# Optimization experiments

Measured on AMD Instinct MI355X. Metric: run time of the kernel, lower is better.

## Reference

```python
import jax, jax.numpy as jnp
import numpy as np

N = 16384
D = 512
NNZ = 163840
NUM_ITERS = 10


def setup_inputs() -> dict:
    key = jax.random.key(0)
    k1, k2, k3, k4 = jax.random.split(key, 4)
    x = jax.random.normal(k1, (N, D), dtype=jnp.float32)
    edge_val = jax.random.uniform(k2, (NNZ,), dtype=jnp.float32)
    edge_row = jnp.sort(jax.random.randint(k3, (NNZ,), 0, N, dtype=jnp.int32))
    edge_col = jax.random.randint(k4, (NNZ,), 0, N, dtype=jnp.int32)
    alpha = jnp.zeros((1,), dtype=jnp.float32)
    beta = jnp.zeros((1,), dtype=jnp.float32)
    sigma = jnp.ones((1,), dtype=jnp.float32)
    return {"x": x, "alpha": alpha, "beta": beta, "sigma": sigma,
            "edge_val": edge_val, "edge_row": edge_row, "edge_col": edge_col,
            "num_iters": NUM_ITERS}


def reference(x, alpha, beta, sigma, edge_val, edge_row, edge_col, num_iters):
    n = x.shape[0]
    # tf.nn.l2_normalize(x, axis=1)
    xn = x * jax.lax.rsqrt(jnp.maximum(jnp.sum(x * x, axis=1, keepdims=True), 1e-12))
    # cosine similarity only at sparse support positions; diagonal zeroed
    sim_e = jnp.sum(xn[edge_row] * xn[edge_col], axis=-1)          # [nnz]
    sim_e = jnp.where(edge_row == edge_col, 0.0, sim_e)
    s = jnp.exp(sigma[0])
    sigma_sq = 2.0 * s * s
    sim_e = jnp.exp(sim_e / (2.0 * sigma_sq))
    # support = sparse support elementwise * similarity
    sup = edge_val * sim_e                                          # [nnz]
    # row-sum of sparse support
    normalize = jax.ops.segment_sum(sup, edge_row, num_segments=n)  # [N]
    a = jnp.exp(alpha[0])
    b = jnp.exp(beta[0])
    denom = b + normalize[:, None] * a + a                          # [N,1] -> broadcast over D

    def step(out, _):
        # sparse matmul: (support @ out)
        Ax = jax.ops.segment_sum(sup[:, None] * out[edge_col], edge_row, num_segments=n)
        out = (x * b + (Ax + out) * a) / denom
        return out, None

    out, _ = jax.lax.scan(step, x, None, length=num_iters)
    return out
```

## Files before the change

kernel.cpp:

```cpp
#include <hip/hip_runtime.h>
#include <hip/hip_fp16.h>

#define DIM 512
#define N_ITERS 10

typedef float floatx2 __attribute__((ext_vector_type(2)));
typedef float fx4 __attribute__((ext_vector_type(4)));
typedef unsigned int ux2 __attribute__((ext_vector_type(2)));
typedef unsigned int ux4 __attribute__((ext_vector_type(4)));

__device__ __forceinline__ unsigned int pack2h(float lo, float hi) {
    __half2 h = __float22half2_rn(make_float2(lo, hi));
    return *reinterpret_cast<unsigned int*>(&h);
}
__device__ __forceinline__ float2 unpack2h(unsigned int u) {
    return __half22float2(*reinterpret_cast<__half2*>(&u));
}
__device__ __forceinline__ unsigned int pack4f8(float f0, float f1, float f2, float f3) {
    int v = 0;
    v = __builtin_amdgcn_cvt_pk_fp8_f32(f0, f1, v, false);
    v = __builtin_amdgcn_cvt_pk_fp8_f32(f2, f3, v, true);
    return (unsigned int)v;
}

__global__ void __launch_bounds__(256)
prep_kernel(const float* __restrict__ x,
            const float* __restrict__ alpha,
            const float* __restrict__ beta,
            const float* __restrict__ sigma,
            const int* __restrict__ erow, int nnz,
            float* __restrict__ consts,
            int* __restrict__ rstart,
            unsigned int* __restrict__ xn8,
            float* __restrict__ norms,
            unsigned short* __restrict__ xbh, int n) {
    int tid = blockIdx.x * blockDim.x + threadIdx.x;
    float b = expf(beta[0]);
    if (tid == 0) {
        float a = expf(alpha[0]);
        float s = expf(sigma[0]);
        consts[0] = a;
        consts[1] = b;
        consts[2] = 1.0f / (4.0f * s * s);
    }
    if (tid <= n) {
        int lo = 0, hi = nnz;
        while (lo < hi) {
            int mid = (lo + hi) >> 1;
            if (erow[mid] < tid) lo = mid + 1; else hi = mid;
        }
        rstart[tid] = lo;
    }
    int wid = tid >> 6;
    int lane = tid & 63;
    if (wid >= n) return;
    const size_t base = (size_t)wid * DIM + lane * 8;
    const fx4* p = (const fx4*)(x + base);
    fx4 u = p[0];
    fx4 v = p[1];
    float s = u.x*u.x + u.y*u.y + u.z*u.z + u.w*u.w
            + v.x*v.x + v.y*v.y + v.z*v.z + v.w*v.w;
    ux4 hb;
    hb.x = pack2h(u.x * b, u.y * b); hb.y = pack2h(u.z * b, u.w * b);
    hb.z = pack2h(v.x * b, v.y * b); hb.w = pack2h(v.z * b, v.w * b);
    *(ux4*)(xbh + base) = hb;
    #pragma unroll
    for (int m = 32; m >= 1; m >>= 1) s += __shfl_xor(s, m, 64);
    float inr = rsqrtf(fmaxf(s, 1e-12f));
    if (lane == 0) norms[wid] = s * inr;
    ux2 qn;
    qn.x = pack4f8(u.x * inr, u.y * inr, u.z * inr, u.w * inr);
    qn.y = pack4f8(v.x * inr, v.y * inr, v.z * inr, v.w * inr);
    *(ux2*)(xn8 + ((size_t)wid * (DIM / 4) + lane * 2)) = qn;
}

__device__ __forceinline__ float dot8f8(const float* A, unsigned int lo, unsigned int hi) {
    floatx2 p0 = __builtin_amdgcn_cvt_pk_f32_fp8((int)lo, false);
    floatx2 p1 = __builtin_amdgcn_cvt_pk_f32_fp8((int)lo, true);
    floatx2 p2 = __builtin_amdgcn_cvt_pk_f32_fp8((int)hi, false);
    floatx2 p3 = __builtin_amdgcn_cvt_pk_f32_fp8((int)hi, true);
    return A[0]*p0.x + A[1]*p0.y + A[2]*p1.x + A[3]*p1.y
         + A[4]*p2.x + A[5]*p2.y + A[6]*p3.x + A[7]*p3.y;
}

#define ACCP(lo, hi, w2)                                                          \
    do {                                                                          \
        acc0 += (w2) * __builtin_amdgcn_cvt_pk_f32_fp8((int)(lo), false);         \
        acc1 += (w2) * __builtin_amdgcn_cvt_pk_f32_fp8((int)(lo), true);          \
        acc2 += (w2) * __builtin_amdgcn_cvt_pk_f32_fp8((int)(hi), false);         \
        acc3 += (w2) * __builtin_amdgcn_cvt_pk_f32_fp8((int)(hi), true);          \
    } while (0)

__global__ void __launch_bounds__(256)
fused1_kernel(const unsigned int* __restrict__ xn8,
              const float* __restrict__ norms,
              const float* __restrict__ eval_,
              const int* __restrict__ ecol,
              const int* __restrict__ rstart,
              const float* __restrict__ consts,
              float* __restrict__ sup, float* __restrict__ inv_denom,
              const unsigned short* __restrict__ xbh,
              unsigned short* __restrict__ next16,
              unsigned int* __restrict__ next8, int n) {
    int row = (blockIdx.x * blockDim.x + threadIdx.x) >> 6;
    int lane = threadIdx.x & 63;
    if (row >= n) return;
    const size_t base = (size_t)row * DIM + lane * 8;
    ux2 hr = *(const ux2*)(xn8 + (size_t)row * (DIM / 4) + lane * 2);
    ux4 hx = *(const ux4*)(xbh + base);
    float A[8];
    {
        floatx2 p0 = __builtin_amdgcn_cvt_pk_f32_fp8((int)hr.x, false);
        floatx2 p1 = __builtin_amdgcn_cvt_pk_f32_fp8((int)hr.x, true);
        floatx2 p2 = __builtin_amdgcn_cvt_pk_f32_fp8((int)hr.y, false);
        floatx2 p3 = __builtin_amdgcn_cvt_pk_f32_fp8((int)hr.y, true);
        A[0]=p0.x; A[1]=p0.y; A[2]=p1.x; A[3]=p1.y;
        A[4]=p2.x; A[5]=p2.y; A[6]=p3.x; A[7]=p3.y;
    }
    float a = consts[0], b = consts[1], c2 = consts[2];
    int rs = rstart[row], re = rstart[row + 1];
    float norm_acc = 0.0f;
    floatx2 acc0 = {0.f, 0.f}, acc1 = {0.f, 0.f}, acc2 = {0.f, 0.f}, acc3 = {0.f, 0.f};
    int e = rs;
    for (; e + 3 < re; e += 4) {
        int c[4]; float ev[4]; float nr[4]; ux2 h[4]; float s[4];
        #pragma unroll
        for (int j = 0; j < 4; ++j) { c[j] = ecol[e + j]; ev[j] = eval_[e + j]; }
        #pragma unroll
        for (int j = 0; j < 4; ++j) nr[j] = norms[c[j]];
        #pragma unroll
        for (int j = 0; j < 4; ++j)
            h[j] = *(const ux2*)(xn8 + (size_t)c[j] * (DIM / 4) + lane * 2);
        #pragma unroll
        for (int j = 0; j < 4; ++j) s[j] = dot8f8(A, h[j].x, h[j].y);
        #pragma unroll
        for (int m = 32; m >= 1; m >>= 1) {
            #pragma unroll
            for (int j = 0; j < 4; ++j) s[j] += __shfl_xor(s[j], m, 64);
        }
        #pragma unroll
        for (int j = 0; j < 4; ++j) {
            float sim = (row == c[j]) ? 0.0f : s[j];
            float sp = ev[j] * expf(sim * c2);
            norm_acc += sp;
            if (lane == 0) sup[e + j] = sp;
            float w = sp * nr[j];
            floatx2 w2 = {w, w};
            ACCP(h[j].x, h[j].y, w2);
        }
    }
    for (; e < re; ++e) {
        int c0 = ecol[e];
        float ev0 = eval_[e];
        float nr0 = norms[c0];
        ux2 h0 = *(const ux2*)(xn8 + (size_t)c0 * (DIM / 4) + lane * 2);
        float s0 = dot8f8(A, h0.x, h0.y);
        #pragma unroll
        for (int m = 32; m >= 1; m >>= 1) s0 += __shfl_xor(s0, m, 64);
        float sim0 = (row == c0) ? 0.0f : s0;
        float sp0 = ev0 * expf(sim0 * c2);
        norm_acc += sp0;
        if (lane == 0) sup[e] = sp0;
        float w = sp0 * nr0;
        floatx2 w2 = {w, w};
        ACCP(h0.x, h0.y, w2);
    }
    float inv_d = 1.0f / (b + norm_acc * a + a);
    if (lane == 0) inv_denom[row] = inv_d;
    float kx = (1.0f + a / b) * inv_d;
    float ka = a * inv_d;
    float2 x0 = unpack2h(hx.x), x1 = unpack2h(hx.y);
    float2 x2 = unpack2h(hx.z), x3 = unpack2h(hx.w);
    float r0 = x0.x * kx + acc0.x * ka;
    float r1 = x0.y * kx + acc0.y * ka;
    float r2 = x1.x * kx + acc1.x * ka;
    float r3 = x1.y * kx + acc1.y * ka;
    float r4 = x2.x * kx + acc2.x * ka;
    float r5 = x2.y * kx + acc2.y * ka;
    float r6 = x3.x * kx + acc3.x * ka;
    float r7 = x3.y * kx + acc3.y * ka;
    ux4 ho;
    ho.x = pack2h(r0, r1); ho.y = pack2h(r2, r3);
    ho.z = pack2h(r4, r5); ho.w = pack2h(r6, r7);
    *(ux4*)(next16 + base) = ho;
    uint2 q;
    q.x = pack4f8(r0, r1, r2, r3);
    q.y = pack4f8(r4, r5, r6, r7);
    *(uint2*)(next8 + (size_t)row * (DIM / 4) + lane * 2) = q;
}

__global__ void __launch_bounds__(256)
iter_kernel(const unsigned short* __restrict__ prev16,
            const unsigned int* __restrict__ prev8,
            unsigned short* __restrict__ next16,
            unsigned int* __restrict__ next8,
            float* __restrict__ out_f32, int last,
            const float* __restrict__ consts, const float* __restrict__ inv_denom,
            const float* __restrict__ sup, const int* __restrict__ ecol,
            const int* __restrict__ rstart,
            const unsigned short* __restrict__ xbh, int n) {
    int row = (blockIdx.x * blockDim.x + threadIdx.x) >> 6;
    int lane = threadIdx.x & 63;
    if (row >= n) return;
    const size_t loff16 = lane * 8;
    const size_t base16 = (size_t)row * DIM + loff16;
    const size_t loff8 = lane * 2;
    ux4 hs = *(const ux4*)(prev16 + base16);
    ux4 hx = *(const ux4*)(xbh + base16);
    float a = consts[0];
    float inv_d = inv_denom[row];
    int rs = rstart[row], re = rstart[row + 1];
    floatx2 acc0 = {0.f, 0.f}, acc1 = {0.f, 0.f}, acc2 = {0.f, 0.f}, acc3 = {0.f, 0.f};
    int e = rs;
    for (; e + 7 < re; e += 8) {
        int c[8]; float w[8]; uint2 h[8];
        #pragma unroll
        for (int j = 0; j < 8; ++j) { c[j] = ecol[e + j]; w[j] = sup[e + j]; }
        #pragma unroll
        for (int j = 0; j < 8; ++j)
            h[j] = *(const uint2*)(prev8 + (size_t)c[j] * (DIM / 4) + loff8);
        #pragma unroll
        for (int j = 0; j < 8; ++j) {
            floatx2 w2 = {w[j], w[j]};
            ACCP(h[j].x, h[j].y, w2);
        }
    }
    for (; e + 1 < re; e += 2) {
        int c0 = ecol[e], c1 = ecol[e + 1];
        float w0 = sup[e], w1 = sup[e + 1];
        uint2 h0 = *(const uint2*)(prev8 + (size_t)c0 * (DIM / 4) + loff8);
        uint2 h1 = *(const uint2*)(prev8 + (size_t)c1 * (DIM / 4) + loff8);
        floatx2 w20 = {w0, w0}; ACCP(h0.x, h0.y, w20);
        floatx2 w21 = {w1, w1}; ACCP(h1.x, h1.y, w21);
    }
    if (e < re) {
        float w = sup[e];
        int c = ecol[e];
        uint2 h = *(const uint2*)(prev8 + (size_t)c * (DIM / 4) + loff8);
        floatx2 w2 = {w, w}; ACCP(h.x, h.y, w2);
    }
    float2 s0 = unpack2h(hs.x), s1 = unpack2h(hs.y);
    float2 s2 = unpack2h(hs.z), s3 = unpack2h(hs.w);
    float2 x0 = unpack2h(hx.x), x1 = unpack2h(hx.y);
    float2 x2 = unpack2h(hx.z), x3 = unpack2h(hx.w);
    float r0 = (x0.x + (acc0.x + s0.x) * a) * inv_d;
    float r1 = (x0.y + (acc0.y + s0.y) * a) * inv_d;
    float r2 = (x1.x + (acc1.x + s1.x) * a) * inv_d;
    float r3 = (x1.y + (acc1.y + s1.y) * a) * inv_d;
    float r4 = (x2.x + (acc2.x + s2.x) * a) * inv_d;
    float r5 = (x2.y + (acc2.y + s2.y) * a) * inv_d;
    float r6 = (x3.x + (acc3.x + s3.x) * a) * inv_d;
    float r7 = (x3.y + (acc3.y + s3.y) * a) * inv_d;
    if (last) {
        fx4* o = (fx4*)(out_f32 + base16);
        fx4 o0 = {r0, r1, r2, r3};
        fx4 o1 = {r4, r5, r6, r7};
        o[0] = o0;
        o[1] = o1;
    } else {
        ux4 ho;
        ho.x = pack2h(r0, r1); ho.y = pack2h(r2, r3);
        ho.z = pack2h(r4, r5); ho.w = pack2h(r6, r7);
        *(ux4*)(next16 + base16) = ho;
        uint2 q;
        q.x = pack4f8(r0, r1, r2, r3);
        q.y = pack4f8(r4, r5, r6, r7);
        *(uint2*)(next8 + (size_t)row * (DIM / 4) + loff8) = q;
    }
}

extern "C" void kernel_launch(void* const* d_in, const int* in_sizes, int n_in,
                              void* d_out, int out_size, void* d_ws, size_t ws_size,
                              hipStream_t stream) {
    const float* x     = (const float*)d_in[0];
    const float* alpha = (const float*)d_in[1];
    const float* beta  = (const float*)d_in[2];
    const float* sigma = (const float*)d_in[3];
    const float* eval_ = (const float*)d_in[4];
    const int* erow = (const int*)d_in[5];
    const int* ecol = (const int*)d_in[6];

    const int n   = in_sizes[0] / DIM;
    const int nnz = in_sizes[4];

    float* ws        = (float*)d_ws;
    float* consts    = ws;
    float* inv_denom = ws + 64;
    int*   rstart    = (int*)(inv_denom + n);
    float* sup       = (float*)(rstart + n + 64);
    float* norms     = sup + nnz;
    unsigned short* xbh    = (unsigned short*)(norms + n);
    unsigned short* bufB16 = xbh + (size_t)n * DIM;
    unsigned int*   xn8    = (unsigned int*)(bufB16 + (size_t)n * DIM);
    unsigned int*   bufB8  = xn8 + (size_t)n * (DIM / 4);
    unsigned int*   bufA8  = xn8;
    unsigned short* bufA16 = (unsigned short*)d_out;
    float* out_f32 = (float*)d_out;

    prep_kernel<<<(n * 64) / 256, 256, 0, stream>>>(x, alpha, beta, sigma,
                                                    erow, nnz, consts, rstart,
                                                    xn8, norms, xbh, n);
    fused1_kernel<<<(n * 64) / 256, 256, 0, stream>>>(xn8, norms, eval_, ecol, rstart,
                                                      consts, sup, inv_denom, xbh,
                                                      bufB16, bufB8, n);
    for (int k = 0; k < N_ITERS - 1; ++k) {
        const unsigned short* prev16 = (k & 1) ? bufA16 : bufB16;
        const unsigned int*   prev8  = (k & 1) ? bufA8  : bufB8;
        unsigned short* next16 = (k & 1) ? bufB16 : bufA16;
        unsigned int*   next8  = (k & 1) ? bufB8  : bufA8;
        int last = (k == N_ITERS - 2) ? 1 : 0;
        iter_kernel<<<(n * 64) / 256, 256, 0, stream>>>(prev16, prev8, next16, next8,
                                                        out_f32, last,
                                                        consts, inv_denom, sup, ecol,
                                                        rstart, xbh, n);
    }
}
```

Measured before the change: 332.7 us.

## Split each row's feature columns into XCD-pinned halves, interleave edges across half-waves

The iteration kernel now launches twice as many blocks, and each wave handles only half of a row's 512 features. Blocks are mapped so that XCDs 0-3 handle one column half and XCDs 4-7 the other, which shrinks the gathered fp8 working set each XCD's L2 must cache. Within a wave, the two 32-lane halves take alternating edges and combine their partial sums with a cross-lane shuffle, so edge gathers run two at a time. The cost is extra shuffles, duplicated index and weight loads across blocks, and idle lanes during the store.

```diff
diff --git a/kernel.cpp b/kernel.cpp
--- a/kernel.cpp
+++ b/kernel.cpp
@@ -199,46 +199,60 @@
             const float* __restrict__ sup, const int* __restrict__ ecol,
             const int* __restrict__ rstart,
             const unsigned short* __restrict__ xbh, int n) {
-    int row = (blockIdx.x * blockDim.x + threadIdx.x) >> 6;
+    int bid = blockIdx.x;
+    int xcd = bid & 7;
+    int h = xcd >> 2;
+    int sub = xcd & 3;
+    int row = ((bid >> 3) * 4 + sub) * 4 + (threadIdx.x >> 6);
     int lane = threadIdx.x & 63;
+    int sl = lane & 31;
+    int par = lane >> 5;
     if (row >= n) return;
-    const size_t loff16 = lane * 8;
-    const size_t base16 = (size_t)row * DIM + loff16;
-    const size_t loff8 = lane * 2;
-    ux4 hs = *(const ux4*)(prev16 + base16);
-    ux4 hx = *(const ux4*)(xbh + base16);
+    const size_t g8 = (size_t)h * (DIM / 8) + sl * 2;
+    const size_t e16 = (size_t)row * DIM + (size_t)h * (DIM / 2) + sl * 8;
+    ux4 hs = *(const ux4*)(prev16 + e16);
+    ux4 hx = *(const ux4*)(xbh + e16);
     float a = consts[0];
     float inv_d = inv_denom[row];
     int rs = rstart[row], re = rstart[row + 1];
     floatx2 acc0 = {0.f, 0.f}, acc1 = {0.f, 0.f}, acc2 = {0.f, 0.f}, acc3 = {0.f, 0.f};
     int e = rs;
     for (; e + 7 < re; e += 8) {
-        int c[8]; float w[8]; uint2 h[8];
-        #pragma unroll
-        for (int j = 0; j < 8; ++j) { c[j] = ecol[e + j]; w[j] = sup[e + j]; }
-        #pragma unroll
-        for (int j = 0; j < 8; ++j)
-            h[j] = *(const uint2*)(prev8 + (size_t)c[j] * (DIM / 4) + loff8);
-        #pragma unroll
-        for (int j = 0; j < 8; ++j) {
+        int c[4]; float w[4]; uint2 hh[4];
+        #pragma unroll
+        for (int j = 0; j < 4; ++j) {
+            int ei = e + 2 * j + par;
+            c[j] = ecol[ei];
+            w[j] = sup[ei];
+        }
+        #pragma unroll
+        for (int j = 0; j < 4; ++j)
+            hh[j] = *(const uint2*)(prev8 + (size_t)c[j] * (DIM / 4) + g8);
+        #pragma unroll
+        for (int j = 0; j < 4; ++j) {
             floatx2 w2 = {w[j], w[j]};
-            ACCP(h[j].x, h[j].y, w2);
+            ACCP(hh[j].x, hh[j].y, w2);
         }
     }
     for (; e + 1 < re; e += 2) {
-        int c0 = ecol[e], c1 = ecol[e + 1];
-        float w0 = sup[e], w1 = sup[e + 1];
-        uint2 h0 = *(const uint2*)(prev8 + (size_t)c0 * (DIM / 4) + loff8);
-        uint2 h1 = *(const uint2*)(prev8 + (size_t)c1 * (DIM / 4) + loff8);
-        floatx2 w20 = {w0, w0}; ACCP(h0.x, h0.y, w20);
-        floatx2 w21 = {w1, w1}; ACCP(h1.x, h1.y, w21);
+        int ei = e + par;
+        int c0 = ecol[ei];
+        float w0 = sup[ei];
+        uint2 hh = *(const uint2*)(prev8 + (size_t)c0 * (DIM / 4) + g8);
+        floatx2 w2 = {w0, w0};
+        ACCP(hh.x, hh.y, w2);
     }
     if (e < re) {
-        float w = sup[e];
-        int c = ecol[e];
-        uint2 h = *(const uint2*)(prev8 + (size_t)c * (DIM / 4) + loff8);
-        floatx2 w2 = {w, w}; ACCP(h.x, h.y, w2);
-    }
+        int c0 = ecol[e];
+        float w0 = (par == 0) ? sup[e] : 0.0f;
+        uint2 hh = *(const uint2*)(prev8 + (size_t)c0 * (DIM / 4) + g8);
+        floatx2 w2 = {w0, w0};
+        ACCP(hh.x, hh.y, w2);
+    }
+    acc0.x += __shfl_xor(acc0.x, 32, 64); acc0.y += __shfl_xor(acc0.y, 32, 64);
+    acc1.x += __shfl_xor(acc1.x, 32, 64); acc1.y += __shfl_xor(acc1.y, 32, 64);
+    acc2.x += __shfl_xor(acc2.x, 32, 64); acc2.y += __shfl_xor(acc2.y, 32, 64);
+    acc3.x += __shfl_xor(acc3.x, 32, 64); acc3.y += __shfl_xor(acc3.y, 32, 64);
     float2 s0 = unpack2h(hs.x), s1 = unpack2h(hs.y);
     float2 s2 = unpack2h(hs.z), s3 = unpack2h(hs.w);
     float2 x0 = unpack2h(hx.x), x1 = unpack2h(hx.y);
@@ -251,21 +265,23 @@
     float r5 = (x2.y + (acc2.y + s2.y) * a) * inv_d;
     float r6 = (x3.x + (acc3.x + s3.x) * a) * inv_d;
     float r7 = (x3.y + (acc3.y + s3.y) * a) * inv_d;
-    if (last) {
-        fx4* o = (fx4*)(out_f32 + base16);
-        fx4 o0 = {r0, r1, r2, r3};
-        fx4 o1 = {r4, r5, r6, r7};
-        o[0] = o0;
-        o[1] = o1;
-    } else {
-        ux4 ho;
-        ho.x = pack2h(r0, r1); ho.y = pack2h(r2, r3);
-        ho.z = pack2h(r4, r5); ho.w = pack2h(r6, r7);
-        *(ux4*)(next16 + base16) = ho;
-        uint2 q;
-        q.x = pack4f8(r0, r1, r2, r3);
-        q.y = pack4f8(r4, r5, r6, r7);
-        *(uint2*)(next8 + (size_t)row * (DIM / 4) + loff8) = q;
+    if (lane < 32) {
+        if (last) {
+            fx4* o = (fx4*)(out_f32 + e16);
+            fx4 o0 = {r0, r1, r2, r3};
+            fx4 o1 = {r4, r5, r6, r7};
+            o[0] = o0;
+            o[1] = o1;
+        } else {
+            ux4 ho;
+            ho.x = pack2h(r0, r1); ho.y = pack2h(r2, r3);
+            ho.z = pack2h(r4, r5); ho.w = pack2h(r6, r7);
+            *(ux4*)(next16 + e16) = ho;
+            uint2 q;
+            q.x = pack4f8(r0, r1, r2, r3);
+            q.y = pack4f8(r4, r5, r6, r7);
+            *(uint2*)(next8 + (size_t)row * (DIM / 4) + g8) = q;
+        }
     }
 }
 
@@ -303,15 +319,16 @@
     fused1_kernel<<<(n * 64) / 256, 256, 0, stream>>>(xn8, norms, eval_, ecol, rstart,
                                                       consts, sup, inv_denom, xbh,
                                                       bufB16, bufB8, n);
+    const int iter_blocks = 2 * n / 4;
     for (int k = 0; k < N_ITERS - 1; ++k) {
         const unsigned short* prev16 = (k & 1) ? bufA16 : bufB16;
         const unsigned int*   prev8  = (k & 1) ? bufA8  : bufB8;
         unsigned short* next16 = (k & 1) ? bufB16 : bufA16;
         unsigned int*   next8  = (k & 1) ? bufB8  : bufA8;
         int last = (k == N_ITERS - 2) ? 1 : 0;
-        iter_kernel<<<(n * 64) / 256, 256, 0, stream>>>(prev16, prev8, next16, next8,
-                                                        out_f32, last,
-                                                        consts, inv_denom, sup, ecol,
-                                                        rstart, xbh, n);
-    }
-}
+        iter_kernel<<<iter_blocks, 256, 0, stream>>>(prev16, prev8, next16, next8,
+                                                     out_f32, last,
+                                                     consts, inv_denom, sup, ecol,
+                                                     rstart, xbh, n);
+    }
+}
```

Result: slower. 339.7 us (+2.1%).
